# Performance work log

Hardware: AMD Instinct MI355X
Metric: run time of the kernel (lower is better)

## Reference

```python
import jax, jax.numpy as jnp
import numpy as np

B, M, N, DIM, P, Q, OUT = 8, 128, 128, 3, 3, 3, 512


def setup_inputs() -> dict:
    key = jax.random.key(0)
    k1, k2, k3, k4, k5 = jax.random.split(key, 5)
    # homogeneous control points [B, m, n, dim+1]; last channel is the NURBS weight w
    ctrl_pts = jax.random.uniform(k1, (B, M, N, DIM + 1), dtype=jnp.float32)
    ctrl_pts = ctrl_pts.at[..., DIM].add(0.5)  # keep weights bounded away from 0
    # knot-span indices per (u,v) grid point: uspan in [P, M-1], vspan in [Q, N-1]
    uspan_uv = jax.random.randint(k2, (OUT, OUT), 0, M - P) + P
    vspan_uv = jax.random.randint(k3, (OUT, OUT), 0, N - Q) + Q
    # precomputed B-spline basis values [OUT, OUT, degree+1]
    Nu_uv = jax.random.uniform(k4, (OUT, OUT, P + 1), dtype=jnp.float32)
    Nv_uv = jax.random.uniform(k5, (OUT, OUT, Q + 1), dtype=jnp.float32)
    return {"ctrl_pts": ctrl_pts, "Nu_uv": Nu_uv, "Nv_uv": Nv_uv,
            "uspan_uv": uspan_uv, "vspan_uv": vspan_uv}


def reference(ctrl_pts, Nu_uv, Nv_uv, uspan_uv, vspan_uv):
    p = Nu_uv.shape[-1] - 1
    q = Nv_uv.shape[-1] - 1
    # control-point index windows: [U, V, p+1] and [U, V, q+1]
    iu = uspan_uv[..., None] - p + jnp.arange(p + 1)
    iv = vspan_uv[..., None] - q + jnp.arange(q + 1)
    # gather local (p+1)x(q+1) control-point patch per eval point:
    # [B, U, V, p+1, q+1, dim+1]
    patch = ctrl_pts[:, iu[:, :, :, None], iv[:, :, None, :], :]
    # basis-weighted sum over local patch (homogeneous coords)
    sw = jnp.einsum('buvlrc,uvl,uvr->buvc', patch, Nu_uv, Nv_uv)
    # rational (perspective) divide by weight channel
    return sw[..., :-1] / sw[..., -1:]
```

## Files before the change

### kernel.cpp

```cpp
#include <hip/hip_runtime.h>
#include <hip/hip_fp16.h>


#define OUTD 512
#define UVN  (OUTD * OUTD)
#define MD   128
#define ND   128
#define BD   8
#define MN   (MD * ND)
#define TPB  1024
#define NCHUNK 32
#define UVPC (UVN / NCHUNK)
#define ITERS (UVPC / TPB)

__device__ __forceinline__ uint2 pack4h(const float4 c) {
    __half2 h01 = __floats2half2_rn(c.x, c.y);
    __half2 h23 = __floats2half2_rn(c.z, c.w);
    uint2 u;
    u.x = *reinterpret_cast<unsigned int*>(&h01);
    u.y = *reinterpret_cast<unsigned int*>(&h23);
    return u;
}

__global__ __launch_bounds__(TPB) void surfeval_r12_kernel(
    const float4* __restrict__ ctrl,
    const float4* __restrict__ Nu4,
    const float4* __restrict__ Nv4,
    const int* __restrict__ uspan,
    const int* __restrict__ vspan,
    float* __restrict__ out)
{
    __shared__ uint2 cl[MN];

    const int bid = blockIdx.x;
    const int b   = (bid >> 3) & 7;
    const int c   = (bid & 7) | ((bid >> 6) << 3);
    const int tid = threadIdx.x;

    const float4* cb = ctrl + b * MN;
    #pragma unroll
    for (int i = 0; i < MN / TPB; ++i) {
        const int idx = i * TPB + tid;
        cl[idx] = pack4h(cb[idx]);
    }
    __syncthreads();

    const char* ldsb = (const char*)cl;

    #pragma unroll 1
    for (int it = 0; it < ITERS; ++it) {
        const int uv = c * UVPC + it * TPB + tid;

        const int us3 = uspan[uv] - 3;
        const int vs3 = vspan[uv] - 3;
        const float4 nu = Nu4[uv];
        const float4 nv = Nv4[uv];

        __half2 nus[4];
        nus[0] = __float2half2_rn(nu.x);
        nus[1] = __float2half2_rn(nu.y);
        nus[2] = __float2half2_rn(nu.z);
        nus[3] = __float2half2_rn(nu.w);
        const float nvL[4] = {nv.x, nv.y, nv.z, nv.w};

        const int base = (us3 * ND + vs3) * 8;
        __half2 t01[4], t23[4];
        #pragma unroll
        for (int r = 0; r < 4; ++r) {
            t01[r] = __float2half2_rn(0.f);
            t23[r] = __float2half2_rn(0.f);
        }
        #pragma unroll
        for (int l = 0; l < 4; ++l) {
            #pragma unroll
            for (int r = 0; r < 4; ++r) {
                const uint2 h = *(const uint2*)(ldsb + base + l * (ND * 8) + r * 8);
                t01[r] = __hfma2(nus[l], *(const __half2*)(&h.x), t01[r]);
                t23[r] = __hfma2(nus[l], *(const __half2*)(&h.y), t23[r]);
            }
        }

        float ax = 0.f, ay = 0.f, az = 0.f, aw = 0.f;
        #pragma unroll
        for (int r = 0; r < 4; ++r) {
            const float2 xy = __half22float2(t01[r]);
            const float2 zw = __half22float2(t23[r]);
            ax = fmaf(nvL[r], xy.x, ax);
            ay = fmaf(nvL[r], xy.y, ay);
            az = fmaf(nvL[r], zw.x, az);
            aw = fmaf(nvL[r], zw.y, aw);
        }

        const float inv = 1.0f / aw;
        float* o = out + ((size_t)b * UVN + uv) * 3;
        o[0] = ax * inv;
        o[1] = ay * inv;
        o[2] = az * inv;
    }
}

extern "C" void kernel_launch(void* const* d_in, const int* in_sizes, int n_in,
                              void* d_out, int out_size, void* d_ws, size_t ws_size,
                              hipStream_t stream) {
    const float* ctrl  = (const float*)d_in[0];
    const float* Nu    = (const float*)d_in[1];
    const float* Nv    = (const float*)d_in[2];
    const int*   uspan = (const int*)d_in[3];
    const int*   vspan = (const int*)d_in[4];
    float* out = (float*)d_out;

    surfeval_r12_kernel<<<NCHUNK * BD, TPB, 0, stream>>>(
        (const float4*)ctrl, (const float4*)Nu, (const float4*)Nv,
        uspan, vspan, out);
}
```

Baseline: 24.46 us.

## Split control grid rows across two blocks and prefetch next iteration inputs

```diff
diff --git a/kernel.cpp b/kernel.cpp
--- a/kernel.cpp
+++ b/kernel.cpp
@@ -12,6 +12,8 @@
 #define NCHUNK 32
 #define UVPC (UVN / NCHUNK)
 #define ITERS (UVPC / TPB)
+#define USPLIT 62
+#define ROWS1  66
 
 __device__ __forceinline__ uint2 pack4h(const float4 c) {
     __half2 h01 = __floats2half2_rn(c.x, c.y);
@@ -22,7 +24,7 @@
     return u;
 }
 
-__global__ __launch_bounds__(TPB) void surfeval_r12_kernel(
+__global__ __launch_bounds__(TPB, 8) void surfeval_r13_kernel(
     const float4* __restrict__ ctrl,
     const float4* __restrict__ Nu4,
     const float4* __restrict__ Nv4,
@@ -30,72 +32,90 @@
     const int* __restrict__ vspan,
     float* __restrict__ out)
 {
-    __shared__ uint2 cl[MN];
+    __shared__ uint2 cl[ROWS1 * ND];
 
     const int bid = blockIdx.x;
-    const int b   = (bid >> 3) & 7;
-    const int c   = (bid & 7) | ((bid >> 6) << 3);
+    const int g   = bid >> 3;
+    const int b   = g & 7;
+    const int h   = (g >> 3) & 1;
+    const int c   = (bid & 7) | ((g >> 4) << 3);
     const int tid = threadIdx.x;
 
-    const float4* cb = ctrl + b * MN;
-    #pragma unroll
-    for (int i = 0; i < MN / TPB; ++i) {
-        const int idx = i * TPB + tid;
-        cl[idx] = pack4h(cb[idx]);
-    }
+    const int row0  = h ? USPLIT : 0;
+    const int nrows = h ? (MD - USPLIT) : (USPLIT + 3);
+    const int nel   = nrows * ND;
+
+    const float4* cb = ctrl + (size_t)b * MN + row0 * ND;
+    for (int i = tid; i < nel; i += TPB)
+        cl[i] = pack4h(cb[i]);
     __syncthreads();
 
     const char* ldsb = (const char*)cl;
 
+    int uv  = c * UVPC + tid;
+    int us3 = uspan[uv] - 3;
+    int vs3 = vspan[uv] - 3;
+    float4 nu = Nu4[uv];
+    float4 nv = Nv4[uv];
+
     #pragma unroll 1
     for (int it = 0; it < ITERS; ++it) {
-        const int uv = c * UVPC + it * TPB + tid;
+        const int   uvC  = uv;
+        const int   us3C = us3, vs3C = vs3;
+        const float4 nuC = nu,  nvC  = nv;
 
-        const int us3 = uspan[uv] - 3;
-        const int vs3 = vspan[uv] - 3;
-        const float4 nu = Nu4[uv];
-        const float4 nv = Nv4[uv];
+        if (it + 1 < ITERS) {
+            const int uvN = uvC + TPB;
+            us3 = uspan[uvN] - 3;
+            vs3 = vspan[uvN] - 3;
+            nu  = Nu4[uvN];
+            nv  = Nv4[uvN];
+            uv  = uvN;
+        }
 
-        __half2 nus[4];
-        nus[0] = __float2half2_rn(nu.x);
-        nus[1] = __float2half2_rn(nu.y);
-        nus[2] = __float2half2_rn(nu.z);
-        nus[3] = __float2half2_rn(nu.w);
-        const float nvL[4] = {nv.x, nv.y, nv.z, nv.w};
+        const bool active = h ? (us3C >= USPLIT) : (us3C < USPLIT);
+        if (active) {
+            __half2 nus[4];
+            nus[0] = __float2half2_rn(nuC.x);
+            nus[1] = __float2half2_rn(nuC.y);
+            nus[2] = __float2half2_rn(nuC.z);
+            nus[3] = __float2half2_rn(nuC.w);
+            const float nvL[4] = {nvC.x, nvC.y, nvC.z, nvC.w};
 
-        const int base = (us3 * ND + vs3) * 8;
-        __half2 t01[4], t23[4];
-        #pragma unroll
-        for (int r = 0; r < 4; ++r) {
-            t01[r] = __float2half2_rn(0.f);
-            t23[r] = __float2half2_rn(0.f);
-        }
-        #pragma unroll
-        for (int l = 0; l < 4; ++l) {
+            const int base = ((us3C - row0) * ND + vs3C) * 8;
+            __half2 t01[4], t23[4];
             #pragma unroll
             for (int r = 0; r < 4; ++r) {
-                const uint2 h = *(const uint2*)(ldsb + base + l * (ND * 8) + r * 8);
-                t01[r] = __hfma2(nus[l], *(const __half2*)(&h.x), t01[r]);
-                t23[r] = __hfma2(nus[l], *(const __half2*)(&h.y), t23[r]);
+                t01[r] = __float2half2_rn(0.f);
+                t23[r] = __float2half2_rn(0.f);
             }
+            #pragma unroll
+            for (int l = 0; l < 4; ++l) {
+                #pragma unroll
+                for (int r = 0; r < 4; ++r) {
+                    const uint2 hh = *(const uint2*)(ldsb + base + l * (ND * 8) + r * 8);
+                    t01[r] = __hfma2(nus[l], *(const __half2*)(&hh.x), t01[r]);
+                    t23[r] = __hfma2(nus[l], *(const __half2*)(&hh.y), t23[r]);
+                }
+            }
+
+            float ax = 0.f, ay = 0.f, az = 0.f, aw = 0.f;
+            #pragma unroll
+            for (int r = 0; r < 4; ++r) {
+                const float2 xy = __half22float2(t01[r]);
+                const float2 zw = __half22float2(t23[r]);
+                ax = fmaf(nvL[r], xy.x, ax);
+                ay = fmaf(nvL[r], xy.y, ay);
+                az = fmaf(nvL[r], zw.x, az);
+                aw = fmaf(nvL[r], zw.y, aw);
+            }
+
+            const float inv = 1.0f / aw;
+            float* o = out + ((size_t)b * UVN + uvC) * 3;
+            o[0] = ax * inv;
+            o[1] = ay * inv;
+            o[2] = az * inv;
         }
-
-        float ax = 0.f, ay = 0.f, az = 0.f, aw = 0.f;
-        #pragma unroll
-        for (int r = 0; r < 4; ++r) {
-            const float2 xy = __half22float2(t01[r]);
-            const float2 zw = __half22float2(t23[r]);
-            ax = fmaf(nvL[r], xy.x, ax);
-            ay = fmaf(nvL[r], xy.y, ay);
-            az = fmaf(nvL[r], zw.x, az);
-            aw = fmaf(nvL[r], zw.y, aw);
-        }
-
-        const float inv = 1.0f / aw;
-        float* o = out + ((size_t)b * UVN + uv) * 3;
-        o[0] = ax * inv;
-        o[1] = ay * inv;
-        o[2] = az * inv;
     }
 }
 
@@ -109,7 +129,7 @@
     const int*   vspan = (const int*)d_in[4];
     float* out = (float*)d_out;
 
-    surfeval_r12_kernel<<<NCHUNK * BD, TPB, 0, stream>>>(
+    surfeval_r13_kernel<<<NCHUNK * BD * 2, TPB, 0, stream>>>(
         (const float4*)ctrl, (const float4*)Nu, (const float4*)Nv,
         uspan, vspan, out);
 }
```

Measured after the change: 27.35 us. +11.8%, slower.
